# Performance work log

Hardware: AMD Instinct MI355X
Metric: run time of the kernel (lower is better)

The kernel has to match this reference:

```python
import jax, jax.numpy as jnp
import numpy as np

M, B, E, A = 3, 65536, 512, 256  # modalities, batch, embedding_dim, attention_dim
LN_EPS = 1e-5


def setup_inputs() -> dict:
    key = jax.random.key(0)
    ks = jax.random.split(key, 9)
    s_e = 1.0 / np.sqrt(E)
    s_a = 1.0 / np.sqrt(A)
    return {
        "x": jax.random.normal(ks[0], (M, B, E), jnp.float32),
        "Wq": jax.random.normal(ks[1], (M, E, A), jnp.float32) * s_e,
        "bq": jax.random.normal(ks[2], (M, A), jnp.float32) * s_e,
        "Wk": jax.random.normal(ks[3], (M, E, A), jnp.float32) * s_e,
        "bk": jax.random.normal(ks[4], (M, A), jnp.float32) * s_e,
        "v": jax.random.normal(ks[5], (M, A), jnp.float32) * s_a,
        "Wt": jax.random.normal(ks[6], (M, M, E, E), jnp.float32) * s_e,
        "bt": jax.random.normal(ks[7], (M, M, E), jnp.float32) * s_e,
        "gamma": jnp.ones((M * E,), jnp.float32),
        "beta": jnp.zeros((M * E,), jnp.float32),
    }


def reference(x, Wq, bq, Wk, bk, v, Wt, bt, gamma, beta):
    # Per-modality query/key projections (batched over modality axis m).
    qp = jnp.einsum('mbe,mea->mba', x, Wq) + bq[:, None, :]  # [M,B,A]
    kp = jnp.einsum('mbe,mea->mba', x, Wk) + bk[:, None, :]  # [M,B,A]
    # Additive score: v_q^T tanh(q_proj[q] + k_proj[k]) for every (q,k) pair.
    t = jnp.tanh(qp[:, None, :, :] + kp[None, :, :, :])       # [Q,K,B,A]
    scores = jnp.einsum('qa,qkba->qkb', v, t)                  # [Q,K,B]
    # Exclude k == q from the softmax (torch code skips key_mod == query_mod).
    diag = jnp.eye(scores.shape[0], dtype=bool)[:, :, None]
    scores = jnp.where(diag, -jnp.inf, scores)
    alpha = jax.nn.softmax(scores, axis=1)                     # [Q,K,B], zero on diag
    # Weighted sum of per-pair linear transforms of the key embeddings.
    att = (jnp.einsum('qkb,kbe,qkef->qbf', alpha, x, Wt)
           + jnp.einsum('qkb,qke->qbe', alpha, bt))            # [Q,B,E]
    attended = x + att                                         # residual per modality
    # Concat modalities along features, then LayerNorm over M*E.
    fused = jnp.transpose(attended, (1, 0, 2)).reshape(x.shape[1], -1)  # [B, M*E]
    mu = jnp.mean(fused, axis=-1, keepdims=True)
    var = jnp.var(fused, axis=-1, keepdims=True)
    fused = (fused - mu) * jax.lax.rsqrt(var + LN_EPS) * gamma + beta
    return fused
```

## Files before the change

kernel.cpp:

```cpp
#include <hip/hip_runtime.h>
#include <hip/hip_bf16.h>

#define MOD   3
#define BATCH 65536
#define EDIM  512
#define ADIM  256
#define FEAT  1536

typedef __attribute__((ext_vector_type(8))) short   s16x8;
typedef __attribute__((ext_vector_type(8))) __bf16  bf16x8;
typedef __attribute__((ext_vector_type(4))) float   f32x4;
typedef __attribute__((ext_vector_type(4))) unsigned short u16x4;

__device__ __forceinline__ float b2f(unsigned short u) {
    union { unsigned int ui; float f; } c; c.ui = ((unsigned int)u) << 16; return c.f;
}
__device__ __forceinline__ unsigned short f2b(float f) {
    __hip_bfloat16 h = __float2bfloat16(f);
    return __builtin_bit_cast(unsigned short, h);
}

__device__ __forceinline__ void glds16(const unsigned short* g, unsigned short* l) {
    __builtin_amdgcn_global_load_lds(
        (const __attribute__((address_space(1))) void*)g,
        (__attribute__((address_space(3))) void*)l, 16, 0, 0);
}

__global__ __launch_bounds__(256) void k_convert_x(const float* __restrict__ x,
                                                   unsigned short* __restrict__ xb, int n4) {
    int i = blockIdx.x * blockDim.x + threadIdx.x;
    int stride = gridDim.x * blockDim.x;
    for (; i < n4; i += stride) {
        f32x4 v = *((const f32x4*)x + i);
        u16x4 o;
        for (int j = 0; j < 4; ++j) o[j] = f2b(v[j]);
        *((u16x4*)xb + i) = o;
    }
}

__global__ __launch_bounds__(256) void k_prep_w(const float* __restrict__ Wq,
                                                const float* __restrict__ Wk,
                                                const float* __restrict__ Wt,
                                                unsigned short* __restrict__ wqk,
                                                unsigned short* __restrict__ wtt2) {
    int i = blockIdx.x * blockDim.x + threadIdx.x;
    int stride = gridDim.x * blockDim.x;
    for (int idx = i; idx < MOD * EDIM * EDIM; idx += stride) {
        int m = idx / (EDIM * EDIM); int r = idx % (EDIM * EDIM);
        int n = r / EDIM; int e = r % EDIM;
        float f = (n < ADIM) ? Wq[(m * EDIM + e) * ADIM + n]
                             : Wk[(m * EDIM + e) * ADIM + (n - ADIM)];
        wqk[idx] = f2b(f);
    }
    for (int idx = i; idx < MOD * 1024 * EDIM; idx += stride) {
        int k = idx / (1024 * EDIM); int r = idx % (1024 * EDIM);
        int n = r / EDIM; int e = r % EDIM;
        int q = (n < EDIM) ? (k + 1) % 3 : (k + 2) % 3;
        int f = (n < EDIM) ? n : n - EDIM;
        wtt2[idx] = f2b(Wt[((size_t)(q * 3 + k) * EDIM + e) * EDIM + f]);
    }
}

#define BM  128
#define BN  128
#define BK  32

__device__ __forceinline__ int swz4(int row) { return (row ^ (row >> 2)) & 3; }

__device__ __forceinline__ void gemm_k512(const unsigned short* __restrict__ Ag,
                                          const unsigned short* __restrict__ Bg,
                                          unsigned short* __restrict__ As,
                                          unsigned short* __restrict__ Bs,
                                          f32x4 (&acc)[4][4]) {
    const int t = threadIdx.x, lane = t & 63, wid = t >> 6;
    const int wr = (wid >> 1) * 64, wc = (wid & 1) * 64;

    const int r0 = wid * 16 + (lane >> 2);
    const int r1 = r0 + 64;
    const int g0 = (lane & 3) ^ swz4(r0);
    const int g1 = (lane & 3) ^ swz4(r1);
    const unsigned short* gA0 = Ag + (size_t)r0 * EDIM + g0 * 8;
    const unsigned short* gA1 = Ag + (size_t)r1 * EDIM + g1 * 8;
    const unsigned short* gB0 = Bg + (size_t)r0 * EDIM + g0 * 8;
    const unsigned short* gB1 = Bg + (size_t)r1 * EDIM + g1 * 8;
    unsigned short* lA0 = As + wid * 512;
    unsigned short* lA1 = As + 2048 + wid * 512;
    unsigned short* lB0 = Bs + wid * 512;
    unsigned short* lB1 = Bs + 2048 + wid * 512;

    const int rr = lane & 15, cg = lane >> 4;
    const unsigned short* aAdr[4];
    const unsigned short* bAdr[4];
#pragma unroll
    for (int i = 0; i < 4; ++i) {
        int ra = wr + i * 16 + rr;
        aAdr[i] = As + ra * BK + ((cg ^ swz4(ra)) * 8);
        int rb = wc + i * 16 + rr;
        bAdr[i] = Bs + rb * BK + ((cg ^ swz4(rb)) * 8);
    }

    for (int kk = 0; kk < EDIM / BK; ++kk) {
        glds16(gA0, lA0); glds16(gA1, lA1);
        glds16(gB0, lB0); glds16(gB1, lB1);
        gA0 += BK; gA1 += BK; gB0 += BK; gB1 += BK;
        __syncthreads();
        s16x8 af[4], bfr[4];
#pragma unroll
        for (int i = 0; i < 4; ++i) af[i]  = *(const s16x8*)aAdr[i];
#pragma unroll
        for (int j = 0; j < 4; ++j) bfr[j] = *(const s16x8*)bAdr[j];
#pragma unroll
        for (int i = 0; i < 4; ++i)
#pragma unroll
            for (int j = 0; j < 4; ++j)
                acc[i][j] = __builtin_amdgcn_mfma_f32_16x16x32_bf16(
                    __builtin_bit_cast(bf16x8, af[i]), __builtin_bit_cast(bf16x8, bfr[j]),
                    acc[i][j], 0, 0, 0);
        __syncthreads();
    }
}

__global__ __launch_bounds__(256) void k_gemm_proj(const unsigned short* __restrict__ xb,
                                                   const unsigned short* __restrict__ wqk,
                                                   const float* __restrict__ bq,
                                                   const float* __restrict__ bk,
                                                   unsigned short* __restrict__ proj) {
    __shared__ __align__(16) unsigned short As[BM * BK];
    __shared__ __align__(16) unsigned short Bs[BN * BK];
    int l = (blockIdx.x & 7) * 768 + (blockIdx.x >> 3);
    int ct = l & 3, rt = (l >> 2) & 511, m = l >> 11;
    int row0 = rt * BM, col0 = ct * BN;
    f32x4 acc[4][4];
#pragma unroll
    for (int i = 0; i < 4; ++i) for (int j = 0; j < 4; ++j) acc[i][j] = (f32x4)0.f;
    gemm_k512(xb + ((size_t)m * BATCH + row0) * EDIM,
              wqk + ((size_t)m * EDIM + col0) * EDIM, As, Bs, acc);
    int lane = threadIdx.x & 63, wid = threadIdx.x >> 6;
    int wr = (wid >> 1) * 64, wc = (wid & 1) * 64;
#pragma unroll
    for (int j = 0; j < 4; ++j) {
        int col = col0 + wc + j * 16 + (lane & 15);
        float bias = (col < ADIM) ? bq[m * ADIM + col] : bk[m * ADIM + col - ADIM];
#pragma unroll
        for (int i = 0; i < 4; ++i) {
            int rbase = row0 + wr + i * 16 + (lane >> 4) * 4;
#pragma unroll
            for (int r = 0; r < 4; ++r)
                proj[((size_t)m * BATCH + rbase + r) * EDIM + col] = f2b(acc[i][j][r] + bias);
        }
    }
}

__global__ __launch_bounds__(256) void k_scores(const unsigned short* __restrict__ proj,
                                                const float* __restrict__ v,
                                                float* __restrict__ alpha) {
    int wid = threadIdx.x >> 6, lane = threadIdx.x & 63;
    size_t b = (size_t)blockIdx.x * 4 + wid;
    float qp[3][4], kp[3][4], vq[3][4];
    for (int m = 0; m < 3; ++m) {
        const unsigned short* p = proj + ((size_t)m * BATCH + b) * EDIM;
        u16x4 uq = *(const u16x4*)(p + lane * 4);
        u16x4 uk = *(const u16x4*)(p + ADIM + lane * 4);
        f32x4 vv = *((const f32x4*)(v + m * ADIM) + lane);
        for (int j = 0; j < 4; ++j) { qp[m][j] = b2f(uq[j]); kp[m][j] = b2f(uk[j]); vq[m][j] = vv[j]; }
    }
    for (int q = 0; q < 3; ++q) {
        float s[2];
        for (int ki = 0; ki < 2; ++ki) {
            int k = (q + 1 + ki) % 3;
            float a = 0.f;
            for (int j = 0; j < 4; ++j) a += vq[q][j] * tanhf(qp[q][j] + kp[k][j]);
            for (int off = 32; off; off >>= 1) a += __shfl_xor(a, off, 64);
            s[ki] = a;
        }
        if (lane == 0) {
            float mx = fmaxf(s[0], s[1]);
            float e0 = expf(s[0] - mx), e1 = expf(s[1] - mx);
            float inv = 1.f / (e0 + e1);
            alpha[(size_t)(q * 2 + 0) * BATCH + b] = e0 * inv;
            alpha[(size_t)(q * 2 + 1) * BATCH + b] = e1 * inv;
        }
    }
}

__global__ __launch_bounds__(256) void k_gemm_y(const unsigned short* __restrict__ xb,
                                                const unsigned short* __restrict__ wtt2,
                                                unsigned short* __restrict__ y) {
    __shared__ __align__(16) unsigned short As[BM * BK];
    __shared__ __align__(16) unsigned short Bs[BN * BK];
    int l = (blockIdx.x & 7) * 1536 + (blockIdx.x >> 3);
    int ct = l & 7, rt = (l >> 3) & 511, k = l >> 12;
    int row0 = rt * BM, col0 = ct * BN;
    f32x4 acc[4][4];
#pragma unroll
    for (int i = 0; i < 4; ++i) for (int j = 0; j < 4; ++j) acc[i][j] = (f32x4)0.f;
    gemm_k512(xb  + ((size_t)k * BATCH + row0) * EDIM,
              wtt2 + ((size_t)k * 1024 + col0) * EDIM, As, Bs, acc);
    int lane = threadIdx.x & 63, wid = threadIdx.x >> 6;
    int wr = (wid >> 1) * 64, wc = (wid & 1) * 64;
    int p   = (ct < 4) ? (((k + 1) % 3) * 2 + 1) : (((k + 2) % 3) * 2 + 0);
    int cb  = (ct < 4) ? col0 : (col0 - EDIM);
#pragma unroll
    for (int j = 0; j < 4; ++j) {
        int col = cb + wc + j * 16 + (lane & 15);
#pragma unroll
        for (int i = 0; i < 4; ++i) {
            int rbase = row0 + wr + i * 16 + (lane >> 4) * 4;
#pragma unroll
            for (int r = 0; r < 4; ++r)
                y[((size_t)p * BATCH + rbase + r) * EDIM + col] = f2b(acc[i][j][r]);
        }
    }
}

__global__ __launch_bounds__(192) void k_fuse_ln(const float* __restrict__ x,
                                                 const unsigned short* __restrict__ y,
                                                 const float* __restrict__ alpha,
                                                 const float* __restrict__ bt,
                                                 const float* __restrict__ gamma,
                                                 const float* __restrict__ beta,
                                                 float* __restrict__ out) {
    __shared__ float red[2][3];
    int b = blockIdx.x, t = threadIdx.x, m = t >> 6, lane = t & 63;
    int e0 = lane * 8;
    float a0 = alpha[(size_t)(m * 2 + 0) * BATCH + b];
    float a1 = alpha[(size_t)(m * 2 + 1) * BATCH + b];
    const float* xp = x + ((size_t)m * BATCH + b) * EDIM + e0;
    f32x4 xv0 = *(const f32x4*)xp, xv1 = *(const f32x4*)(xp + 4);
    s16x8 y0 = *(const s16x8*)(y + ((size_t)(m * 2 + 0) * BATCH + b) * EDIM + e0);
    s16x8 y1 = *(const s16x8*)(y + ((size_t)(m * 2 + 1) * BATCH + b) * EDIM + e0);
    int kA = (m + 1) % 3, kB = (m + 2) % 3;
    const float* bA = bt + (size_t)(m * 3 + kA) * EDIM + e0;
    const float* bB = bt + (size_t)(m * 3 + kB) * EDIM + e0;
    f32x4 bA0 = *(const f32x4*)bA, bA1 = *(const f32x4*)(bA + 4);
    f32x4 bB0 = *(const f32x4*)bB, bB1 = *(const f32x4*)(bB + 4);
    float v[8]; float s = 0.f, s2 = 0.f;
#pragma unroll
    for (int j = 0; j < 8; ++j) {
        float xx = (j < 4) ? xv0[j] : xv1[j - 4];
        float ba = (j < 4) ? bA0[j] : bA1[j - 4];
        float bb = (j < 4) ? bB0[j] : bB1[j - 4];
        float vv = xx + a0 * (b2f((unsigned short)y0[j]) + ba)
                      + a1 * (b2f((unsigned short)y1[j]) + bb);
        v[j] = vv; s += vv; s2 += vv * vv;
    }
    for (int off = 32; off; off >>= 1) { s += __shfl_xor(s, off, 64); s2 += __shfl_xor(s2, off, 64); }
    if (lane == 0) { red[0][m] = s; red[1][m] = s2; }
    __syncthreads();
    float S = red[0][0] + red[0][1] + red[0][2];
    float S2 = red[1][0] + red[1][1] + red[1][2];
    float mu  = S * (1.f / 1536.f);
    float var = S2 * (1.f / 1536.f) - mu * mu;
    float rs  = rsqrtf(var + 1e-5f);
    int f0 = m * EDIM + e0;
    f32x4 g0 = *(const f32x4*)(gamma + f0), g1 = *(const f32x4*)(gamma + f0 + 4);
    f32x4 be0 = *(const f32x4*)(beta + f0), be1 = *(const f32x4*)(beta + f0 + 4);
    f32x4 o0, o1;
#pragma unroll
    for (int j = 0; j < 4; ++j) {
        o0[j] = (v[j]     - mu) * rs * g0[j] + be0[j];
        o1[j] = (v[j + 4] - mu) * rs * g1[j] + be1[j];
    }
    float* op = out + (size_t)b * FEAT + f0;
    *(f32x4*)op = o0; *(f32x4*)(op + 4) = o1;
}

extern "C" void kernel_launch(void* const* d_in, const int* in_sizes, int n_in,
                              void* d_out, int out_size, void* d_ws, size_t ws_size,
                              hipStream_t stream) {
    const float* x     = (const float*)d_in[0];
    const float* Wq    = (const float*)d_in[1];
    const float* bq    = (const float*)d_in[2];
    const float* Wk    = (const float*)d_in[3];
    const float* bk    = (const float*)d_in[4];
    const float* v     = (const float*)d_in[5];
    const float* Wt    = (const float*)d_in[6];
    const float* bt    = (const float*)d_in[7];
    const float* gamma = (const float*)d_in[8];
    const float* beta  = (const float*)d_in[9];
    float* out = (float*)d_out;

    char* ws = (char*)d_ws;
    unsigned short* wqk   = (unsigned short*)(ws);
    unsigned short* wtt2  = (unsigned short*)(ws + 1572864);
    float*          alpha = (float*)        (ws + 4718592);
    unsigned short* xb    = (unsigned short*)(ws + 6291456);
    unsigned short* y     = (unsigned short*)(ws + 207618048);
    unsigned short* proj  = y;

    k_convert_x<<<4096, 256, 0, stream>>>(x, xb, (MOD * BATCH * EDIM) / 4);
    k_prep_w   <<<2048, 256, 0, stream>>>(Wq, Wk, Wt, wqk, wtt2);
    k_gemm_proj<<<6144, 256, 0, stream>>>(xb, wqk, bq, bk, proj);
    k_scores   <<<16384, 256, 0, stream>>>(proj, v, alpha);
    k_gemm_y   <<<12288, 256, 0, stream>>>(xb, wtt2, y);
    k_fuse_ln  <<<65536, 192, 0, stream>>>(x, y, alpha, bt, gamma, beta, out);
}
```

Baseline: 912.5 us.

## Triple-buffer GEMM LDS loads and read bf16 x in fused LayerNorm

Both projection GEMMs get a three-stage LDS ring, so global-to-LDS loads for the next two K tiles overlap the MFMA work on the current tile. This replaces the old load-sync-compute-sync loop, and waits are now tracked with explicit vmcnt counts. The MFMA block is also wrapped in s_setprio to raise the wave's priority. Separately, the fused LayerNorm kernel now reads the residual x from the bf16 copy instead of fp32, halving that traffic at some cost in residual precision. The triple buffer raises LDS per block from 16KB to 48KB, which may lower occupancy.

Result: slower. 990.7 us (+8.6%).

```diff
diff --git a/kernel.cpp b/kernel.cpp
--- a/kernel.cpp
+++ b/kernel.cpp
@@ -64,60 +64,96 @@
 #define BM  128
 #define BN  128
 #define BK  32
+#define NKT 16
+#define BUFE 4096
 
 __device__ __forceinline__ int swz4(int row) { return (row ^ (row >> 2)) & 3; }
 
-__device__ __forceinline__ void gemm_k512(const unsigned short* __restrict__ Ag,
-                                          const unsigned short* __restrict__ Bg,
-                                          unsigned short* __restrict__ As,
-                                          unsigned short* __restrict__ Bs,
-                                          f32x4 (&acc)[4][4]) {
+struct PipeCtx {
+    const unsigned short *gA0, *gA1, *gB0, *gB1;
+    unsigned short *As, *Bs;
+    int lo0, lo1;
+    int offA[4], offB[4];
+};
+
+__device__ __forceinline__ void pipe_init(PipeCtx& c,
+                                          const unsigned short* Ag, const unsigned short* Bg,
+                                          unsigned short* As, unsigned short* Bs) {
     const int t = threadIdx.x, lane = t & 63, wid = t >> 6;
     const int wr = (wid >> 1) * 64, wc = (wid & 1) * 64;
-
-    const int r0 = wid * 16 + (lane >> 2);
-    const int r1 = r0 + 64;
-    const int g0 = (lane & 3) ^ swz4(r0);
-    const int g1 = (lane & 3) ^ swz4(r1);
-    const unsigned short* gA0 = Ag + (size_t)r0 * EDIM + g0 * 8;
-    const unsigned short* gA1 = Ag + (size_t)r1 * EDIM + g1 * 8;
-    const unsigned short* gB0 = Bg + (size_t)r0 * EDIM + g0 * 8;
-    const unsigned short* gB1 = Bg + (size_t)r1 * EDIM + g1 * 8;
-    unsigned short* lA0 = As + wid * 512;
-    unsigned short* lA1 = As + 2048 + wid * 512;
-    unsigned short* lB0 = Bs + wid * 512;
-    unsigned short* lB1 = Bs + 2048 + wid * 512;
-
+    const int r0 = wid * 16 + (lane >> 2), r1 = r0 + 64;
+    c.gA0 = Ag + (size_t)r0 * EDIM + (((lane & 3) ^ swz4(r0)) * 8);
+    c.gA1 = Ag + (size_t)r1 * EDIM + (((lane & 3) ^ swz4(r1)) * 8);
+    c.gB0 = Bg + (size_t)r0 * EDIM + (((lane & 3) ^ swz4(r0)) * 8);
+    c.gB1 = Bg + (size_t)r1 * EDIM + (((lane & 3) ^ swz4(r1)) * 8);
+    c.As = As; c.Bs = Bs;
+    c.lo0 = wid * 512; c.lo1 = 2048 + wid * 512;
     const int rr = lane & 15, cg = lane >> 4;
-    const unsigned short* aAdr[4];
-    const unsigned short* bAdr[4];
 #pragma unroll
     for (int i = 0; i < 4; ++i) {
         int ra = wr + i * 16 + rr;
-        aAdr[i] = As + ra * BK + ((cg ^ swz4(ra)) * 8);
+        c.offA[i] = ra * BK + ((cg ^ swz4(ra)) * 8);
         int rb = wc + i * 16 + rr;
-        bAdr[i] = Bs + rb * BK + ((cg ^ swz4(rb)) * 8);
-    }
-
-    for (int kk = 0; kk < EDIM / BK; ++kk) {
-        glds16(gA0, lA0); glds16(gA1, lA1);
-        glds16(gB0, lB0); glds16(gB1, lB1);
-        gA0 += BK; gA1 += BK; gB0 += BK; gB1 += BK;
-        __syncthreads();
-        s16x8 af[4], bfr[4];
-#pragma unroll
-        for (int i = 0; i < 4; ++i) af[i]  = *(const s16x8*)aAdr[i];
-#pragma unroll
-        for (int j = 0; j < 4; ++j) bfr[j] = *(const s16x8*)bAdr[j];
-#pragma unroll
-        for (int i = 0; i < 4; ++i)
-#pragma unroll
-            for (int j = 0; j < 4; ++j)
-                acc[i][j] = __builtin_amdgcn_mfma_f32_16x16x32_bf16(
-                    __builtin_bit_cast(bf16x8, af[i]), __builtin_bit_cast(bf16x8, bfr[j]),
-                    acc[i][j], 0, 0, 0);
-        __syncthreads();
-    }
+        c.offB[i] = rb * BK + ((cg ^ swz4(rb)) * 8);
+    }
+}
+
+__device__ __forceinline__ void pipe_stage(const PipeCtx& c, int kt, int buf) {
+    glds16(c.gA0 + kt * BK, c.As + buf * BUFE + c.lo0);
+    glds16(c.gA1 + kt * BK, c.As + buf * BUFE + c.lo1);
+    glds16(c.gB0 + kt * BK, c.Bs + buf * BUFE + c.lo0);
+    glds16(c.gB1 + kt * BK, c.Bs + buf * BUFE + c.lo1);
+}
+
+__device__ __forceinline__ void pipe_compute(const PipeCtx& c, int buf, f32x4 (&acc)[4][4]) {
+    const unsigned short* ab = c.As + buf * BUFE;
+    const unsigned short* bb = c.Bs + buf * BUFE;
+    s16x8 af[4], bfr[4];
+#pragma unroll
+    for (int i = 0; i < 4; ++i) af[i]  = *(const s16x8*)(ab + c.offA[i]);
+#pragma unroll
+    for (int j = 0; j < 4; ++j) bfr[j] = *(const s16x8*)(bb + c.offB[j]);
+    __builtin_amdgcn_s_setprio(1);
+#pragma unroll
+    for (int i = 0; i < 4; ++i)
+#pragma unroll
+        for (int j = 0; j < 4; ++j)
+            acc[i][j] = __builtin_amdgcn_mfma_f32_16x16x32_bf16(
+                __builtin_bit_cast(bf16x8, af[i]), __builtin_bit_cast(bf16x8, bfr[j]),
+                acc[i][j], 0, 0, 0);
+    __builtin_amdgcn_s_setprio(0);
+}
+
+__device__ __forceinline__ void gemm_pipe_k512(const unsigned short* __restrict__ Ag,
+                                               const unsigned short* __restrict__ Bg,
+                                               unsigned short* __restrict__ As,
+                                               unsigned short* __restrict__ Bs,
+                                               f32x4 (&acc)[4][4]) {
+    PipeCtx c;
+    pipe_init(c, Ag, Bg, As, Bs);
+    pipe_stage(c, 0, 0);
+    pipe_stage(c, 1, 1);
+    asm volatile("s_waitcnt vmcnt(4)" ::: "memory");
+    __builtin_amdgcn_s_barrier();
+    int bc = 0, bn = 2;
+#pragma unroll 1
+    for (int kt = 0; kt < NKT - 2; ++kt) {
+        pipe_stage(c, kt + 2, bn);
+        asm volatile("s_waitcnt vmcnt(8)" ::: "memory");
+        __builtin_amdgcn_s_barrier();
+        pipe_compute(c, bc, acc);
+        __builtin_amdgcn_s_barrier();
+        bc = (bc == 2) ? 0 : bc + 1;
+        bn = (bn == 2) ? 0 : bn + 1;
+    }
+    asm volatile("s_waitcnt vmcnt(4)" ::: "memory");
+    __builtin_amdgcn_s_barrier();
+    pipe_compute(c, bc, acc);
+    __builtin_amdgcn_s_barrier();
+    bc = (bc == 2) ? 0 : bc + 1;
+    asm volatile("s_waitcnt vmcnt(0)" ::: "memory");
+    __builtin_amdgcn_s_barrier();
+    pipe_compute(c, bc, acc);
 }
 
 __global__ __launch_bounds__(256) void k_gemm_proj(const unsigned short* __restrict__ xb,
@@ -125,16 +161,16 @@
                                                    const float* __restrict__ bq,
                                                    const float* __restrict__ bk,
                                                    unsigned short* __restrict__ proj) {
-    __shared__ __align__(16) unsigned short As[BM * BK];
-    __shared__ __align__(16) unsigned short Bs[BN * BK];
+    __shared__ __align__(16) unsigned short As[3 * BUFE];
+    __shared__ __align__(16) unsigned short Bs[3 * BUFE];
     int l = (blockIdx.x & 7) * 768 + (blockIdx.x >> 3);
     int ct = l & 3, rt = (l >> 2) & 511, m = l >> 11;
     int row0 = rt * BM, col0 = ct * BN;
     f32x4 acc[4][4];
 #pragma unroll
     for (int i = 0; i < 4; ++i) for (int j = 0; j < 4; ++j) acc[i][j] = (f32x4)0.f;
-    gemm_k512(xb + ((size_t)m * BATCH + row0) * EDIM,
-              wqk + ((size_t)m * EDIM + col0) * EDIM, As, Bs, acc);
+    gemm_pipe_k512(xb + ((size_t)m * BATCH + row0) * EDIM,
+                   wqk + ((size_t)m * EDIM + col0) * EDIM, As, Bs, acc);
     int lane = threadIdx.x & 63, wid = threadIdx.x >> 6;
     int wr = (wid >> 1) * 64, wc = (wid & 1) * 64;
 #pragma unroll
@@ -186,20 +222,20 @@
 __global__ __launch_bounds__(256) void k_gemm_y(const unsigned short* __restrict__ xb,
                                                 const unsigned short* __restrict__ wtt2,
                                                 unsigned short* __restrict__ y) {
-    __shared__ __align__(16) unsigned short As[BM * BK];
-    __shared__ __align__(16) unsigned short Bs[BN * BK];
+    __shared__ __align__(16) unsigned short As[3 * BUFE];
+    __shared__ __align__(16) unsigned short Bs[3 * BUFE];
     int l = (blockIdx.x & 7) * 1536 + (blockIdx.x >> 3);
     int ct = l & 7, rt = (l >> 3) & 511, k = l >> 12;
     int row0 = rt * BM, col0 = ct * BN;
     f32x4 acc[4][4];
 #pragma unroll
     for (int i = 0; i < 4; ++i) for (int j = 0; j < 4; ++j) acc[i][j] = (f32x4)0.f;
-    gemm_k512(xb  + ((size_t)k * BATCH + row0) * EDIM,
-              wtt2 + ((size_t)k * 1024 + col0) * EDIM, As, Bs, acc);
+    gemm_pipe_k512(xb + ((size_t)k * BATCH + row0) * EDIM,
+                   wtt2 + ((size_t)k * 1024 + col0) * EDIM, As, Bs, acc);
     int lane = threadIdx.x & 63, wid = threadIdx.x >> 6;
     int wr = (wid >> 1) * 64, wc = (wid & 1) * 64;
-    int p   = (ct < 4) ? (((k + 1) % 3) * 2 + 1) : (((k + 2) % 3) * 2 + 0);
-    int cb  = (ct < 4) ? col0 : (col0 - EDIM);
+    int p  = (ct < 4) ? (((k + 1) % 3) * 2 + 1) : (((k + 2) % 3) * 2 + 0);
+    int cb = (ct < 4) ? col0 : (col0 - EDIM);
 #pragma unroll
     for (int j = 0; j < 4; ++j) {
         int col = cb + wc + j * 16 + (lane & 15);
@@ -213,7 +249,7 @@
     }
 }
 
-__global__ __launch_bounds__(192) void k_fuse_ln(const float* __restrict__ x,
+__global__ __launch_bounds__(192) void k_fuse_ln(const unsigned short* __restrict__ xb,
                                                  const unsigned short* __restrict__ y,
                                                  const float* __restrict__ alpha,
                                                  const float* __restrict__ bt,
@@ -225,8 +261,7 @@
     int e0 = lane * 8;
     float a0 = alpha[(size_t)(m * 2 + 0) * BATCH + b];
     float a1 = alpha[(size_t)(m * 2 + 1) * BATCH + b];
-    const float* xp = x + ((size_t)m * BATCH + b) * EDIM + e0;
-    f32x4 xv0 = *(const f32x4*)xp, xv1 = *(const f32x4*)(xp + 4);
+    s16x8 xv = *(const s16x8*)(xb + ((size_t)m * BATCH + b) * EDIM + e0);
     s16x8 y0 = *(const s16x8*)(y + ((size_t)(m * 2 + 0) * BATCH + b) * EDIM + e0);
     s16x8 y1 = *(const s16x8*)(y + ((size_t)(m * 2 + 1) * BATCH + b) * EDIM + e0);
     int kA = (m + 1) % 3, kB = (m + 2) % 3;
@@ -237,11 +272,10 @@
     float v[8]; float s = 0.f, s2 = 0.f;
 #pragma unroll
     for (int j = 0; j < 8; ++j) {
-        float xx = (j < 4) ? xv0[j] : xv1[j - 4];
         float ba = (j < 4) ? bA0[j] : bA1[j - 4];
         float bb = (j < 4) ? bB0[j] : bB1[j - 4];
-        float vv = xx + a0 * (b2f((unsigned short)y0[j]) + ba)
-                      + a1 * (b2f((unsigned short)y1[j]) + bb);
+        float vv = b2f((unsigned short)xv[j]) + a0 * (b2f((unsigned short)y0[j]) + ba)
+                                             + a1 * (b2f((unsigned short)y1[j]) + bb);
         v[j] = vv; s += vv; s2 += vv * vv;
     }
     for (int off = 32; off; off >>= 1) { s += __shfl_xor(s, off, 64); s2 += __shfl_xor(s2, off, 64); }
@@ -293,5 +327,5 @@
     k_gemm_proj<<<6144, 256, 0, stream>>>(xb, wqk, bq, bk, proj);
     k_scores   <<<16384, 256, 0, stream>>>(proj, v, alpha);
     k_gemm_y   <<<12288, 256, 0, stream>>>(xb, wtt2, y);
-    k_fuse_ln  <<<65536, 192, 0, stream>>>(x, y, alpha, bt, gamma, beta, out);
-}
+    k_fuse_ln  <<<65536, 192, 0, stream>>>(xb, y, alpha, bt, gamma, beta, out);
+}
```

## Rewrite GEMMs as 256x256 tiles with multi-stage async LDS pipeline

Applied to the files above, without the earlier changes.

Replaces the 128x128 single-buffered GEMM core with a 256x256 tile per 512-thread block. Global-to-LDS loads are prefetched several stages ahead, with explicit vmcnt waits, raw barriers and s_setprio around the MFMA bursts, so load latency overlaps compute and there is more reuse per byte loaded. The fused LayerNorm kernel now reads the bf16 copy of x instead of the fp32 input, which halves that traffic but adds rounding error to the residual. The large tile raises register and LDS pressure per block.

Result: no change. 899.7 us (-1.4%).

```diff
diff --git a/kernel.cpp b/kernel.cpp
--- a/kernel.cpp
+++ b/kernel.cpp
@@ -24,6 +24,13 @@
     __builtin_amdgcn_global_load_lds(
         (const __attribute__((address_space(1))) void*)g,
         (__attribute__((address_space(3))) void*)l, 16, 0, 0);
+}
+
+#define WAITV(N) asm volatile("s_waitcnt vmcnt(%0)" :: "i"(N) : "memory")
+__device__ __forceinline__ void BAR() {
+    asm volatile("" ::: "memory");
+    __builtin_amdgcn_s_barrier();
+    asm volatile("" ::: "memory");
 }
 
 __global__ __launch_bounds__(256) void k_convert_x(const float* __restrict__ x,
@@ -61,92 +68,117 @@
     }
 }
 
-#define BM  128
-#define BN  128
-#define BK  32
-
-__device__ __forceinline__ int swz4(int row) { return (row ^ (row >> 2)) & 3; }
-
-__device__ __forceinline__ void gemm_k512(const unsigned short* __restrict__ Ag,
-                                          const unsigned short* __restrict__ Bg,
-                                          unsigned short* __restrict__ As,
-                                          unsigned short* __restrict__ Bs,
-                                          f32x4 (&acc)[4][4]) {
-    const int t = threadIdx.x, lane = t & 63, wid = t >> 6;
-    const int wr = (wid >> 1) * 64, wc = (wid & 1) * 64;
-
-    const int r0 = wid * 16 + (lane >> 2);
-    const int r1 = r0 + 64;
-    const int g0 = (lane & 3) ^ swz4(r0);
-    const int g1 = (lane & 3) ^ swz4(r1);
-    const unsigned short* gA0 = Ag + (size_t)r0 * EDIM + g0 * 8;
-    const unsigned short* gA1 = Ag + (size_t)r1 * EDIM + g1 * 8;
-    const unsigned short* gB0 = Bg + (size_t)r0 * EDIM + g0 * 8;
-    const unsigned short* gB1 = Bg + (size_t)r1 * EDIM + g1 * 8;
-    unsigned short* lA0 = As + wid * 512;
-    unsigned short* lA1 = As + 2048 + wid * 512;
-    unsigned short* lB0 = Bs + wid * 512;
-    unsigned short* lB1 = Bs + 2048 + wid * 512;
-
-    const int rr = lane & 15, cg = lane >> 4;
-    const unsigned short* aAdr[4];
-    const unsigned short* bAdr[4];
-#pragma unroll
-    for (int i = 0; i < 4; ++i) {
-        int ra = wr + i * 16 + rr;
-        aAdr[i] = As + ra * BK + ((cg ^ swz4(ra)) * 8);
-        int rb = wc + i * 16 + rr;
-        bAdr[i] = Bs + rb * BK + ((cg ^ swz4(rb)) * 8);
-    }
-
-    for (int kk = 0; kk < EDIM / BK; ++kk) {
-        glds16(gA0, lA0); glds16(gA1, lA1);
-        glds16(gB0, lB0); glds16(gB1, lB1);
-        gA0 += BK; gA1 += BK; gB0 += BK; gB1 += BK;
-        __syncthreads();
-        s16x8 af[4], bfr[4];
-#pragma unroll
-        for (int i = 0; i < 4; ++i) af[i]  = *(const s16x8*)aAdr[i];
-#pragma unroll
-        for (int j = 0; j < 4; ++j) bfr[j] = *(const s16x8*)bAdr[j];
-#pragma unroll
-        for (int i = 0; i < 4; ++i)
-#pragma unroll
-            for (int j = 0; j < 4; ++j)
-                acc[i][j] = __builtin_amdgcn_mfma_f32_16x16x32_bf16(
-                    __builtin_bit_cast(bf16x8, af[i]), __builtin_bit_cast(bf16x8, bfr[j]),
-                    acc[i][j], 0, 0, 0);
-        __syncthreads();
-    }
-}
-
-__global__ __launch_bounds__(256) void k_gemm_proj(const unsigned short* __restrict__ xb,
-                                                   const unsigned short* __restrict__ wqk,
-                                                   const float* __restrict__ bq,
-                                                   const float* __restrict__ bk,
-                                                   unsigned short* __restrict__ proj) {
-    __shared__ __align__(16) unsigned short As[BM * BK];
-    __shared__ __align__(16) unsigned short Bs[BN * BK];
-    int l = (blockIdx.x & 7) * 768 + (blockIdx.x >> 3);
-    int ct = l & 3, rt = (l >> 2) & 511, m = l >> 11;
-    int row0 = rt * BM, col0 = ct * BN;
-    f32x4 acc[4][4];
-#pragma unroll
-    for (int i = 0; i < 4; ++i) for (int j = 0; j < 4; ++j) acc[i][j] = (f32x4)0.f;
-    gemm_k512(xb + ((size_t)m * BATCH + row0) * EDIM,
-              wqk + ((size_t)m * EDIM + col0) * EDIM, As, Bs, acc);
+
+struct GCtx {
+    const unsigned short* pA;
+    const unsigned short* pB;
+    const unsigned short* lds;
+    unsigned short* ldsW;
+    int aoff, boff;
+};
+
+__device__ __forceinline__ void stage_s(const GCtx& c, int s) {
+    if (s >= 32) return;
+    int colK = (s >> 2) * 64 + (s & 2) * 16;
+    const unsigned short* src = ((s & 1) ? c.pB : c.pA) + colK;
+    unsigned short* dst = c.ldsW + (s & 7) * 8192;
+    glds16(src, dst);
+    glds16(src + 16 * 512, dst + 512);
+}
+
+template<int Q>
+__device__ __forceinline__ void phase_compute(int T, const GCtx& c,
+                                              s16x8 (&bfr)[4], f32x4 (&acc)[8][4]) {
+    constexpr int ks = Q >> 1, rh = Q & 1;
+    const unsigned short* Asl = c.lds + ((T & 1) * 4 + 2 * ks) * 8192;
+    const unsigned short* Bsl = Asl + 8192;
+    s16x8 af[4];
+#pragma unroll
+    for (int i = 0; i < 4; ++i) af[i] = *(const s16x8*)(Asl + c.aoff + (rh * 4 + i) * 512);
+    if constexpr ((Q & 1) == 0) {
+#pragma unroll
+        for (int j = 0; j < 4; ++j) bfr[j] = *(const s16x8*)(Bsl + c.boff + j * 512);
+    }
+    __builtin_amdgcn_s_setprio(1);
+#pragma unroll
+    for (int i = 0; i < 4; ++i)
+#pragma unroll
+        for (int j = 0; j < 4; ++j)
+            acc[rh * 4 + i][j] = __builtin_amdgcn_mfma_f32_16x16x32_bf16(
+                __builtin_bit_cast(bf16x8, af[i]), __builtin_bit_cast(bf16x8, bfr[j]),
+                acc[rh * 4 + i][j], 0, 0, 0);
+    __builtin_amdgcn_s_setprio(0);
+}
+
+template<int W0, int W2>
+__device__ __forceinline__ void do_tile(int T, const GCtx& c,
+                                        s16x8 (&bfr)[4], f32x4 (&acc)[8][4]) {
+    stage_s(c, 4 * T + 6);
+    WAITV(W0); BAR();
+    phase_compute<0>(T, c, bfr, acc);
+    BAR();
+    stage_s(c, 4 * T + 7);
+    phase_compute<1>(T, c, bfr, acc);
+    BAR();
+    stage_s(c, 4 * T + 8);
+    WAITV(W2); BAR();
+    phase_compute<2>(T, c, bfr, acc);
+    BAR();
+    stage_s(c, 4 * T + 9);
+    phase_compute<3>(T, c, bfr, acc);
+    BAR();
+}
+
+__device__ __forceinline__ void gemm256_core(const unsigned short* Ag,
+                                             const unsigned short* Bg,
+                                             unsigned short* lds, f32x4 (&acc)[8][4]) {
+    const int tid = threadIdx.x, lane = tid & 63, wid = tid >> 6;
+    const int wm = wid >> 2, wn = wid & 3;
+    GCtx c;
+    int stageRow = wid * 32 + (lane >> 2);
+    int gsrc8 = ((lane & 3) ^ ((lane >> 3) & 3)) * 8;
+    c.pA = Ag + (size_t)stageRow * 512 + gsrc8;
+    c.pB = Bg + (size_t)stageRow * 512 + gsrc8;
+    c.lds = lds;
+    c.ldsW = lds + wid * 1024;
+    int swz8 = ((lane >> 4) ^ ((lane >> 1) & 3)) * 8;
+    c.aoff = (wm * 128 + (lane & 15)) * 32 + swz8;
+    c.boff = (wn * 64 + (lane & 15)) * 32 + swz8;
+    s16x8 bfr[4];
+#pragma unroll
+    for (int s = 0; s < 6; ++s) stage_s(c, s);
+#pragma unroll 1
+    for (int t = 0; t < 6; ++t) do_tile<10, 10>(t, c, bfr, acc);
+    do_tile<10, 8>(6, c, bfr, acc);
+    do_tile<4, 0>(7, c, bfr, acc);
+}
+
+__global__ __launch_bounds__(512, 2) void k_gemm_proj(const unsigned short* __restrict__ xb,
+                                                      const unsigned short* __restrict__ wqk,
+                                                      const float* __restrict__ bq,
+                                                      const float* __restrict__ bk,
+                                                      unsigned short* __restrict__ proj) {
+    __shared__ __align__(16) unsigned short LDS[65536];
+    int l = (blockIdx.x & 7) * 192 + (blockIdx.x >> 3);
+    int ct = l & 1, rt = (l >> 1) & 255, m = l >> 9;
+    int row0 = rt * 256, col0 = ct * 256;
+    f32x4 acc[8][4];
+#pragma unroll
+    for (int i = 0; i < 8; ++i) for (int j = 0; j < 4; ++j) acc[i][j] = (f32x4)0.f;
+    gemm256_core(xb + ((size_t)m * BATCH + row0) * EDIM,
+                 wqk + ((size_t)m * EDIM + col0) * EDIM, LDS, acc);
     int lane = threadIdx.x & 63, wid = threadIdx.x >> 6;
-    int wr = (wid >> 1) * 64, wc = (wid & 1) * 64;
+    int wm = wid >> 2, wn = wid & 3;
 #pragma unroll
     for (int j = 0; j < 4; ++j) {
-        int col = col0 + wc + j * 16 + (lane & 15);
+        int col = col0 + wn * 64 + j * 16 + (lane & 15);
         float bias = (col < ADIM) ? bq[m * ADIM + col] : bk[m * ADIM + col - ADIM];
 #pragma unroll
-        for (int i = 0; i < 4; ++i) {
-            int rbase = row0 + wr + i * 16 + (lane >> 4) * 4;
+        for (int i8 = 0; i8 < 8; ++i8) {
+            int rbase = row0 + wm * 128 + i8 * 16 + (lane >> 4) * 4;
 #pragma unroll
             for (int r = 0; r < 4; ++r)
-                proj[((size_t)m * BATCH + rbase + r) * EDIM + col] = f2b(acc[i][j][r] + bias);
+                proj[((size_t)m * BATCH + rbase + r) * EDIM + col] = f2b(acc[i8][j][r] + bias);
         }
     }
 }
@@ -183,37 +215,36 @@
     }
 }
 
-__global__ __launch_bounds__(256) void k_gemm_y(const unsigned short* __restrict__ xb,
-                                                const unsigned short* __restrict__ wtt2,
-                                                unsigned short* __restrict__ y) {
-    __shared__ __align__(16) unsigned short As[BM * BK];
-    __shared__ __align__(16) unsigned short Bs[BN * BK];
-    int l = (blockIdx.x & 7) * 1536 + (blockIdx.x >> 3);
-    int ct = l & 7, rt = (l >> 3) & 511, k = l >> 12;
-    int row0 = rt * BM, col0 = ct * BN;
-    f32x4 acc[4][4];
-#pragma unroll
-    for (int i = 0; i < 4; ++i) for (int j = 0; j < 4; ++j) acc[i][j] = (f32x4)0.f;
-    gemm_k512(xb  + ((size_t)k * BATCH + row0) * EDIM,
-              wtt2 + ((size_t)k * 1024 + col0) * EDIM, As, Bs, acc);
+__global__ __launch_bounds__(512, 2) void k_gemm_y(const unsigned short* __restrict__ xb,
+                                                   const unsigned short* __restrict__ wtt2,
+                                                   unsigned short* __restrict__ y) {
+    __shared__ __align__(16) unsigned short LDS[65536];
+    int l = (blockIdx.x & 7) * 384 + (blockIdx.x >> 3);
+    int ct = l & 3, rt = (l >> 2) & 255, k = l >> 10;
+    int row0 = rt * 256, col0 = ct * 256;
+    f32x4 acc[8][4];
+#pragma unroll
+    for (int i = 0; i < 8; ++i) for (int j = 0; j < 4; ++j) acc[i][j] = (f32x4)0.f;
+    gemm256_core(xb + ((size_t)k * BATCH + row0) * EDIM,
+                 wtt2 + ((size_t)k * 1024 + col0) * EDIM, LDS, acc);
     int lane = threadIdx.x & 63, wid = threadIdx.x >> 6;
-    int wr = (wid >> 1) * 64, wc = (wid & 1) * 64;
-    int p   = (ct < 4) ? (((k + 1) % 3) * 2 + 1) : (((k + 2) % 3) * 2 + 0);
-    int cb  = (ct < 4) ? col0 : (col0 - EDIM);
+    int wm = wid >> 2, wn = wid & 3;
+    int p  = (ct < 2) ? (((k + 1) % 3) * 2 + 1) : (((k + 2) % 3) * 2 + 0);
+    int cb = (ct < 2) ? col0 : (col0 - EDIM);
 #pragma unroll
     for (int j = 0; j < 4; ++j) {
-        int col = cb + wc + j * 16 + (lane & 15);
-#pragma unroll
-        for (int i = 0; i < 4; ++i) {
-            int rbase = row0 + wr + i * 16 + (lane >> 4) * 4;
+        int col = cb + wn * 64 + j * 16 + (lane & 15);
+#pragma unroll
+        for (int i8 = 0; i8 < 8; ++i8) {
+            int rbase = row0 + wm * 128 + i8 * 16 + (lane >> 4) * 4;
 #pragma unroll
             for (int r = 0; r < 4; ++r)
-                y[((size_t)p * BATCH + rbase + r) * EDIM + col] = f2b(acc[i][j][r]);
+                y[((size_t)p * BATCH + rbase + r) * EDIM + col] = f2b(acc[i8][j][r]);
         }
     }
 }
 
-__global__ __launch_bounds__(192) void k_fuse_ln(const float* __restrict__ x,
+__global__ __launch_bounds__(192) void k_fuse_ln(const unsigned short* __restrict__ xb,
                                                  const unsigned short* __restrict__ y,
                                                  const float* __restrict__ alpha,
                                                  const float* __restrict__ bt,
@@ -225,8 +256,7 @@
     int e0 = lane * 8;
     float a0 = alpha[(size_t)(m * 2 + 0) * BATCH + b];
     float a1 = alpha[(size_t)(m * 2 + 1) * BATCH + b];
-    const float* xp = x + ((size_t)m * BATCH + b) * EDIM + e0;
-    f32x4 xv0 = *(const f32x4*)xp, xv1 = *(const f32x4*)(xp + 4);
+    s16x8 xv = *(const s16x8*)(xb + ((size_t)m * BATCH + b) * EDIM + e0);
     s16x8 y0 = *(const s16x8*)(y + ((size_t)(m * 2 + 0) * BATCH + b) * EDIM + e0);
     s16x8 y1 = *(const s16x8*)(y + ((size_t)(m * 2 + 1) * BATCH + b) * EDIM + e0);
     int kA = (m + 1) % 3, kB = (m + 2) % 3;
@@ -237,11 +267,10 @@
     float v[8]; float s = 0.f, s2 = 0.f;
 #pragma unroll
     for (int j = 0; j < 8; ++j) {
-        float xx = (j < 4) ? xv0[j] : xv1[j - 4];
         float ba = (j < 4) ? bA0[j] : bA1[j - 4];
         float bb = (j < 4) ? bB0[j] : bB1[j - 4];
-        float vv = xx + a0 * (b2f((unsigned short)y0[j]) + ba)
-                      + a1 * (b2f((unsigned short)y1[j]) + bb);
+        float vv = b2f((unsigned short)xv[j]) + a0 * (b2f((unsigned short)y0[j]) + ba)
+                                             + a1 * (b2f((unsigned short)y1[j]) + bb);
         v[j] = vv; s += vv; s2 += vv * vv;
     }
     for (int off = 32; off; off >>= 1) { s += __shfl_xor(s, off, 64); s2 += __shfl_xor(s2, off, 64); }
@@ -290,8 +319,8 @@
 
     k_convert_x<<<4096, 256, 0, stream>>>(x, xb, (MOD * BATCH * EDIM) / 4);
     k_prep_w   <<<2048, 256, 0, stream>>>(Wq, Wk, Wt, wqk, wtt2);
-    k_gemm_proj<<<6144, 256, 0, stream>>>(xb, wqk, bq, bk, proj);
+    k_gemm_proj<<<1536, 512, 0, stream>>>(xb, wqk, bq, bk, proj);
     k_scores   <<<16384, 256, 0, stream>>>(proj, v, alpha);
-    k_gemm_y   <<<12288, 256, 0, stream>>>(xb, wtt2, y);
-    k_fuse_ln  <<<65536, 192, 0, stream>>>(x, y, alpha, bt, gamma, beta, out);
-}
+    k_gemm_y   <<<3072, 512, 0, stream>>>(xb, wtt2, y);
+    k_fuse_ln  <<<65536, 192, 0, stream>>>(xb, y, alpha, bt, gamma, beta, out);
+}
```
